# Optimization experiments

Measured on AMD Instinct MI355X. Metric: run time of the kernel, lower is better.

The kernel has to match this reference:

```python
import jax, jax.numpy as jnp
import numpy as np

B, S, D, H, NH = 4, 4096, 256, 1024, 8


def _layernorm(x, g, b, eps=1e-5):
    mu = jnp.mean(x, axis=-1, keepdims=True)
    var = jnp.var(x, axis=-1, keepdims=True)
    return (x - mu) / jnp.sqrt(var + eps) * g + b


def setup_inputs() -> dict:
    key = jax.random.key(0)
    ks = jax.random.split(key, 3)
    std = 0.02
    return {
        "x": jax.random.normal(ks[0], (B, S, D), dtype=jnp.float32),
        "gamma1": jnp.ones((D,), jnp.float32),
        "beta1": jnp.zeros((D,), jnp.float32),
        "W1": jax.random.normal(ks[1], (D, H), dtype=jnp.float32) * std,
        "b1": jnp.zeros((H,), jnp.float32),
        "W2": jax.random.normal(ks[2], (H, D), dtype=jnp.float32) * std,
        "b2": jnp.zeros((D,), jnp.float32),
        "gamma2": jnp.ones((D,), jnp.float32),
        "beta2": jnp.zeros((D,), jnp.float32),
        "n_head": NH,
    }


def reference(x, gamma1, beta1, W1, b1, W2, b2, gamma2, beta2, n_head):
    # First-call path of CachedLocalMultiheadAttention: single-head softmax
    # attention on raw x, scale = (d_model // n_head) ** -0.5, no masks.
    scale = (x.shape[-1] // n_head) ** -0.5
    scores = jnp.einsum('bqd,bkd->bqk', x, x) * scale  # [B,S,S]
    attn = jax.nn.softmax(scores, axis=-1)
    a = jnp.einsum('bqk,bkd->bqd', attn, x)
    # residual + LayerNorm (dropouts are identity in eval)
    h = _layernorm(a + x, gamma1, beta1)
    # positionwise FFN
    f = jnp.maximum(h @ W1 + b1, 0.0) @ W2 + b2
    return _layernorm(f + h, gamma2, beta2)
```

## Files before the change

kernel.cpp:

```cpp
#include <hip/hip_runtime.h>


#define DIM 256
#define SEQ 4096
#define BATCHN 4
#define HID 1024
#define NROW (BATCHN * SEQ)

typedef __attribute__((ext_vector_type(8))) short short8;
typedef __attribute__((ext_vector_type(4))) float float4v;
typedef __attribute__((ext_vector_type(16))) float float16v;

static __device__ __forceinline__ unsigned int f2bf1(float f) {
  unsigned int b = __float_as_uint(f);
  return (b + 0x7fffu + ((b >> 16) & 1u)) >> 16;
}
static __device__ __forceinline__ unsigned int pack2bf(float lo, float hi) {
  return f2bf1(lo) | (f2bf1(hi) << 16);
}
static __device__ __forceinline__ float bf2f(unsigned short v) {
  return __uint_as_float(((unsigned int)v) << 16);
}
static __device__ __forceinline__ float bflo(unsigned int p) { return __uint_as_float(p << 16); }
static __device__ __forceinline__ float bfhi(unsigned int p) { return __uint_as_float(p & 0xffff0000u); }

static __device__ __forceinline__ void bar_lgkm() {
  __asm__ __volatile__("s_waitcnt lgkmcnt(0)" ::: "memory");
  __builtin_amdgcn_s_barrier();
  __asm__ __volatile__("" ::: "memory");
}

__global__ __launch_bounds__(256, 2) void attn_part(
    const float* __restrict__ x,
    unsigned short* __restrict__ P01, unsigned short* __restrict__ P23,
    float* __restrict__ lpart) {
  __shared__ unsigned short Krow[32][264];
  __shared__ unsigned short Vt[256][40];
  __shared__ unsigned short Pbuf[4][32][40];

  const int tid = threadIdx.x;
  const int w = tid >> 6;
  const int l = tid & 63;
  const int n = l & 31;
  const int half = l >> 5;
  const int b = blockIdx.y;
  const int z = blockIdx.z;
  const int qw = (blockIdx.x << 7) + (w << 5);
  const float* xb = x + (size_t)b * SEQ * DIM;
  const float scale = 0.17677669529663687f;
  const float SHIFT = 46.0f;

  short8 qf[16];
#pragma unroll
  for (int c = 0; c < 16; c++) {
    const float* qp = xb + (size_t)(qw + n) * DIM + (c << 4) + (half << 3);
    float4 a0 = *reinterpret_cast<const float4*>(qp);
    float4 a1 = *reinterpret_cast<const float4*>(qp + 4);
    short8 q8;
    q8[0] = (short)f2bf1(a0.x); q8[1] = (short)f2bf1(a0.y);
    q8[2] = (short)f2bf1(a0.z); q8[3] = (short)f2bf1(a0.w);
    q8[4] = (short)f2bf1(a1.x); q8[5] = (short)f2bf1(a1.y);
    q8[6] = (short)f2bf1(a1.z); q8[7] = (short)f2bf1(a1.w);
    qf[c] = q8;
  }

  float16v o[8];
#pragma unroll
  for (int nb = 0; nb < 8; nb++)
#pragma unroll
    for (int r = 0; r < 16; r++) o[nb][r] = 0.f;
  float lsum = 0.f;

  const int skey = tid & 31;
  const int sd = (tid >> 5) << 5;
  const int kbase = z << 10;

  float4 ld0[4];
  {
    const float* sp = xb + (size_t)(kbase + skey) * DIM + sd;
#pragma unroll
    for (int j = 0; j < 4; j++) ld0[j] = *reinterpret_cast<const float4*>(sp + (j << 2));
  }

  for (int k0 = kbase; k0 < kbase + 1024; k0 += 32) {
    const float* sp = xb + (size_t)(k0 + skey) * DIM + sd;
    float4 ld1[4];
#pragma unroll
    for (int j = 0; j < 4; j++) ld1[j] = *reinterpret_cast<const float4*>(sp + 16 + (j << 2));

    bar_lgkm();
#pragma unroll
    for (int j = 0; j < 4; j++)
      *reinterpret_cast<uint2*>(&Krow[skey][sd + (j << 2)]) =
          make_uint2(pack2bf(ld0[j].x, ld0[j].y), pack2bf(ld0[j].z, ld0[j].w));
#pragma unroll
    for (int j = 0; j < 4; j++)
      *reinterpret_cast<uint2*>(&Krow[skey][sd + 16 + (j << 2)]) =
          make_uint2(pack2bf(ld1[j].x, ld1[j].y), pack2bf(ld1[j].z, ld1[j].w));
#pragma unroll
    for (int j = 0; j < 4; j++) {
      Vt[sd + (j << 2) + 0][skey] = (unsigned short)f2bf1(ld0[j].x);
      Vt[sd + (j << 2) + 1][skey] = (unsigned short)f2bf1(ld0[j].y);
      Vt[sd + (j << 2) + 2][skey] = (unsigned short)f2bf1(ld0[j].z);
      Vt[sd + (j << 2) + 3][skey] = (unsigned short)f2bf1(ld0[j].w);
    }
#pragma unroll
    for (int j = 0; j < 4; j++) {
      Vt[sd + 16 + (j << 2) + 0][skey] = (unsigned short)f2bf1(ld1[j].x);
      Vt[sd + 16 + (j << 2) + 1][skey] = (unsigned short)f2bf1(ld1[j].y);
      Vt[sd + 16 + (j << 2) + 2][skey] = (unsigned short)f2bf1(ld1[j].z);
      Vt[sd + 16 + (j << 2) + 3][skey] = (unsigned short)f2bf1(ld1[j].w);
    }
    bar_lgkm();

    {
      const int kn = (k0 + 32 < kbase + 1024) ? (k0 + 32) : k0;
      const float* spn = xb + (size_t)(kn + skey) * DIM + sd;
#pragma unroll
      for (int j = 0; j < 4; j++) ld0[j] = *reinterpret_cast<const float4*>(spn + (j << 2));
    }

    float16v s;
#pragma unroll
    for (int r = 0; r < 16; r++) s[r] = 0.f;
#pragma unroll
    for (int c = 0; c < 16; c++) {
      short8 a = *reinterpret_cast<const short8*>(&Krow[n][(c << 4) + (half << 3)]);
      s = __builtin_amdgcn_mfma_f32_32x32x16_bf16(a, qf[c], s, 0, 0, 0);
    }
#pragma unroll
    for (int g = 0; g < 4; g++) {
      float p0 = __expf(fmaf(s[(g << 2) + 0], scale, -SHIFT));
      float p1 = __expf(fmaf(s[(g << 2) + 1], scale, -SHIFT));
      float p2 = __expf(fmaf(s[(g << 2) + 2], scale, -SHIFT));
      float p3 = __expf(fmaf(s[(g << 2) + 3], scale, -SHIFT));
      lsum += (p0 + p1) + (p2 + p3);
      *reinterpret_cast<uint2*>(&Pbuf[w][n][(g << 3) + (half << 2)]) =
          make_uint2(pack2bf(p0, p1), pack2bf(p2, p3));
    }
    __asm__ __volatile__("" ::: "memory");

#pragma unroll
    for (int kk = 0; kk < 2; kk++) {
      short8 pf = *reinterpret_cast<const short8*>(&Pbuf[w][n][(kk << 4) + (half << 3)]);
#pragma unroll
      for (int nb = 0; nb < 8; nb++) {
        short8 vf = *reinterpret_cast<const short8*>(&Vt[(nb << 5) + n][(kk << 4) + (half << 3)]);
        o[nb] = __builtin_amdgcn_mfma_f32_32x32x16_bf16(pf, vf, o[nb], 0, 0, 0);
      }
    }
  }

  lsum += __shfl_xor(lsum, 32);
  if (l < 32) lpart[(z << 14) + (b << 12) + qw + l] = lsum;

  unsigned short* Op = ((z < 2) ? P01 : P23) + ((size_t)(z & 1) << 22);
#pragma unroll
  for (int nb = 0; nb < 8; nb++) {
#pragma unroll
    for (int r = 0; r < 16; r++) {
      const int q = (r & 3) + ((r >> 2) << 3) + (half << 2);
      Op[((size_t)(b << 12) + qw + q) * DIM + (nb << 5) + n] = (unsigned short)f2bf1(o[nb][r]);
    }
  }
}

__global__ __launch_bounds__(256) void merge_ln1(
    const unsigned short* __restrict__ P01, const unsigned short* __restrict__ P23,
    const float* __restrict__ lpart, const float* __restrict__ x,
    const float* __restrict__ g1, const float* __restrict__ be1,
    unsigned short* __restrict__ hbf) {
  const int tid = threadIdx.x;
  const int row = (blockIdx.x << 5) + (tid >> 3);
  const int c0 = (tid & 7) << 5;
  const float rl = 1.0f / (lpart[row] + lpart[NROW + row] +
                           lpart[2 * NROW + row] + lpart[3 * NROW + row]);
  const float* px = x + (size_t)row * DIM + c0;

  float v[32];
#pragma unroll
  for (int j = 0; j < 32; j++) v[j] = 0.f;
#pragma unroll
  for (int part = 0; part < 4; part++) {
    const unsigned short* pb = ((part < 2) ? P01 : P23) + ((size_t)(part & 1) << 22) +
                               (size_t)row * DIM + c0;
#pragma unroll
    for (int j = 0; j < 8; j++) {
      uint2 raw = *reinterpret_cast<const uint2*>(pb + (j << 2));
      v[(j << 2) + 0] += bflo(raw.x); v[(j << 2) + 1] += bfhi(raw.x);
      v[(j << 2) + 2] += bflo(raw.y); v[(j << 2) + 3] += bfhi(raw.y);
    }
  }
#pragma unroll
  for (int j = 0; j < 8; j++) {
    float4 xr = *reinterpret_cast<const float4*>(px + (j << 2));
    v[(j << 2) + 0] = fmaf(v[(j << 2) + 0], rl, xr.x);
    v[(j << 2) + 1] = fmaf(v[(j << 2) + 1], rl, xr.y);
    v[(j << 2) + 2] = fmaf(v[(j << 2) + 2], rl, xr.z);
    v[(j << 2) + 3] = fmaf(v[(j << 2) + 3], rl, xr.w);
  }
  float s = 0.f, s2 = 0.f;
#pragma unroll
  for (int j = 0; j < 32; j++) { s += v[j]; s2 = fmaf(v[j], v[j], s2); }
  s += __shfl_xor(s, 1); s += __shfl_xor(s, 2); s += __shfl_xor(s, 4);
  s2 += __shfl_xor(s2, 1); s2 += __shfl_xor(s2, 2); s2 += __shfl_xor(s2, 4);
  const float mean = s * (1.f / 256.f);
  const float var = s2 * (1.f / 256.f) - mean * mean;
  const float rstd = rsqrtf(var + 1e-5f);
  unsigned short* hb = hbf + (size_t)row * DIM + c0;
  unsigned int pk[16];
#pragma unroll
  for (int j = 0; j < 8; j++) {
    float4 gv = *reinterpret_cast<const float4*>(g1 + c0 + (j << 2));
    float4 bv = *reinterpret_cast<const float4*>(be1 + c0 + (j << 2));
    float o0 = fmaf((v[(j << 2) + 0] - mean) * rstd, gv.x, bv.x);
    float o1 = fmaf((v[(j << 2) + 1] - mean) * rstd, gv.y, bv.y);
    float o2 = fmaf((v[(j << 2) + 2] - mean) * rstd, gv.z, bv.z);
    float o3 = fmaf((v[(j << 2) + 3] - mean) * rstd, gv.w, bv.w);
    pk[2 * j] = pack2bf(o0, o1); pk[2 * j + 1] = pack2bf(o2, o3);
  }
#pragma unroll
  for (int q = 0; q < 4; q++)
    *reinterpret_cast<uint4*>(hb + (q << 3)) =
        make_uint4(pk[4 * q], pk[4 * q + 1], pk[4 * q + 2], pk[4 * q + 3]);
}

__global__ __launch_bounds__(256) void prep_w(
    const float* __restrict__ W1, const float* __restrict__ W2,
    unsigned short* __restrict__ W1Tb, unsigned short* __restrict__ W2Tb) {
  __shared__ float Ls[64][65];
  const int tid = threadIdx.x;
  const bool second = blockIdx.x >= 64;
  const int bid = blockIdx.x - (second ? 64 : 0);
  const int N = second ? DIM : HID;
  const float* src = second ? W2 : W1;
  unsigned short* dst = second ? W2Tb : W1Tb;
  const int ntn = N >> 6;
  const int k0 = (bid / ntn) << 6, n0 = (bid % ntn) << 6;

  const int r = tid >> 2, cg = (tid & 3) << 4;
#pragma unroll
  for (int q = 0; q < 4; q++) {
    float4 v = *reinterpret_cast<const float4*>(src + (size_t)(k0 + r) * N + n0 + cg + (q << 2));
    Ls[r][cg + (q << 2) + 0] = v.x; Ls[r][cg + (q << 2) + 1] = v.y;
    Ls[r][cg + (q << 2) + 2] = v.z; Ls[r][cg + (q << 2) + 3] = v.w;
  }
  __syncthreads();
  const int j = tid >> 2, part = tid & 3;
  const int kbl = part >> 1, ko = (part & 1) << 4, kl = part << 4;
  unsigned int pk[8];
#pragma unroll
  for (int q = 0; q < 8; q++) pk[q] = pack2bf(Ls[kl + 2 * q][j], Ls[kl + 2 * q + 1][j]);
  unsigned short* dp = dst + (((size_t)((k0 >> 5) + kbl) * N + n0 + j) << 5) + ko;
  *reinterpret_cast<uint4*>(dp) = make_uint4(pk[0], pk[1], pk[2], pk[3]);
  *reinterpret_cast<uint4*>(dp + 8) = make_uint4(pk[4], pk[5], pk[6], pk[7]);
}

__global__ __launch_bounds__(256) void ffn1_mfma(
    const unsigned short* __restrict__ hbf, const unsigned short* __restrict__ W1Tb,
    const float* __restrict__ b1, unsigned short* __restrict__ ub) {
  __shared__ unsigned short As[128][264];
  __shared__ unsigned short Bs[128][40];
  const int tid = threadIdx.x;
  const int w = tid >> 6;
  const int l = tid & 63;
  const int tx = l & 15;
  const int p = l >> 4;
  const int wm = w >> 1, wn = w & 1;
  const int r0 = blockIdx.x << 7, c0 = blockIdx.y << 7;

  float4v acc[4][4];
#pragma unroll
  for (int i = 0; i < 4; i++)
#pragma unroll
    for (int j = 0; j < 4; j++) acc[i][j] = (float4v){0.f, 0.f, 0.f, 0.f};

  {
    const unsigned short* base = hbf + (size_t)r0 * DIM;
#pragma unroll
    for (int j = 0; j < 16; j++) {
      const int fo = (tid << 3) + (j << 11);
      uint4 v = *reinterpret_cast<const uint4*>(base + fo);
      *reinterpret_cast<uint4*>(&As[fo >> 8][fo & 255]) = v;
    }
  }
  for (int kb = 0; kb < 8; kb++) {
    __syncthreads();
    {
      const unsigned short* base = W1Tb + (((size_t)kb * HID + c0) << 5);
#pragma unroll
      for (int j = 0; j < 2; j++) {
        const int fo = (tid << 3) + (j << 11);
        uint4 v = *reinterpret_cast<const uint4*>(base + fo);
        *reinterpret_cast<uint4*>(&Bs[fo >> 5][fo & 31]) = v;
      }
    }
    __syncthreads();
    short8 af[4], bf[4];
#pragma unroll
    for (int f = 0; f < 4; f++) {
      af[f] = *reinterpret_cast<const short8*>(&As[(wm << 6) + (f << 4) + tx][(kb << 5) + (p << 3)]);
      bf[f] = *reinterpret_cast<const short8*>(&Bs[(wn << 6) + (f << 4) + tx][p << 3]);
    }
#pragma unroll
    for (int i = 0; i < 4; i++)
#pragma unroll
      for (int j = 0; j < 4; j++)
        acc[i][j] = __builtin_amdgcn_mfma_f32_16x16x32_bf16(af[i], bf[j], acc[i][j], 0, 0, 0);
  }
  float bias[4];
#pragma unroll
  for (int j = 0; j < 4; j++) bias[j] = b1[c0 + (wn << 6) + (j << 4) + tx];
  __syncthreads();
  unsigned short (*Ep)[72] = reinterpret_cast<unsigned short(*)[72]>(&As[0][0] + w * 2304);
#pragma unroll
  for (int hh = 0; hh < 2; hh++) {
#pragma unroll
    for (int i2 = 0; i2 < 2; i2++) {
      const int i = (hh << 1) + i2;
#pragma unroll
      for (int j = 0; j < 4; j++)
#pragma unroll
        for (int rg = 0; rg < 4; rg++)
          Ep[(i2 << 4) + (p << 2) + rg][(j << 4) + tx] =
              (unsigned short)f2bf1(fmaxf(acc[i][j][rg] + bias[j], 0.f));
    }
    __syncthreads();
    const int cb = l >> 5, r32 = l & 31;
    const int grow = r0 + (wm << 6) + (hh << 5) + r32;
    const int kb = (c0 >> 5) + (wn << 1) + cb;
    unsigned short* up = ub + (((size_t)kb * NROW + grow) << 5);
#pragma unroll
    for (int q = 0; q < 4; q++)
      *reinterpret_cast<uint4*>(up + (q << 3)) =
          *reinterpret_cast<const uint4*>(&Ep[r32][(cb << 5) + (q << 3)]);
    __syncthreads();
  }
}

__global__ __launch_bounds__(256) void ffn2_mfma(
    const unsigned short* __restrict__ ub, const unsigned short* __restrict__ W2Tb,
    const float* __restrict__ b2, const unsigned short* __restrict__ hbf,
    const float* __restrict__ g2, const float* __restrict__ be2,
    float* __restrict__ out) {
  __shared__ unsigned short As[32][40];
  __shared__ unsigned short Bs[256][40];
  __shared__ float2 red[32][4];
  const int tid = threadIdx.x;
  const int w = tid >> 6;
  const int l = tid & 63;
  const int tx = l & 15;
  const int p = l >> 4;
  const int r0 = blockIdx.x << 5;

  float4v acc[2][4];
#pragma unroll
  for (int i = 0; i < 2; i++)
#pragma unroll
    for (int j = 0; j < 4; j++) acc[i][j] = (float4v){0.f, 0.f, 0.f, 0.f};

  for (int kb = 0; kb < 32; kb++) {
    __syncthreads();
    if (tid < 128) {
      const int fo = tid << 3;
      uint4 v = *reinterpret_cast<const uint4*>(ub + (((size_t)kb * NROW + r0) << 5) + fo);
      *reinterpret_cast<uint4*>(&As[fo >> 5][fo & 31]) = v;
    }
    {
      const unsigned short* base = W2Tb + (((size_t)kb * DIM) << 5);
#pragma unroll
      for (int j = 0; j < 4; j++) {
        const int fo = (tid << 3) + (j << 11);
        uint4 v = *reinterpret_cast<const uint4*>(base + fo);
        *reinterpret_cast<uint4*>(&Bs[fo >> 5][fo & 31]) = v;
      }
    }
    __syncthreads();
    short8 af[2], bf[4];
#pragma unroll
    for (int i = 0; i < 2; i++)
      af[i] = *reinterpret_cast<const short8*>(&As[(i << 4) + tx][p << 3]);
#pragma unroll
    for (int j = 0; j < 4; j++)
      bf[j] = *reinterpret_cast<const short8*>(&Bs[(w << 6) + (j << 4) + tx][p << 3]);
#pragma unroll
    for (int i = 0; i < 2; i++)
#pragma unroll
      for (int j = 0; j < 4; j++)
        acc[i][j] = __builtin_amdgcn_mfma_f32_16x16x32_bf16(af[i], bf[j], acc[i][j], 0, 0, 0);
  }

  float bias[4];
#pragma unroll
  for (int j = 0; j < 4; j++) bias[j] = b2[(w << 6) + (j << 4) + tx];
#pragma unroll
  for (int i = 0; i < 2; i++)
#pragma unroll
    for (int rg = 0; rg < 4; rg++) {
      const int row = r0 + (i << 4) + (p << 2) + rg;
#pragma unroll
      for (int j = 0; j < 4; j++)
        acc[i][j][rg] += bias[j] + bf2f(hbf[(size_t)row * DIM + (w << 6) + (j << 4) + tx]);
    }
#pragma unroll
  for (int i = 0; i < 2; i++)
#pragma unroll
    for (int rg = 0; rg < 4; rg++) {
      float s = acc[i][0][rg] + acc[i][1][rg] + acc[i][2][rg] + acc[i][3][rg];
      float s2 = 0.f;
#pragma unroll
      for (int j = 0; j < 4; j++) s2 = fmaf(acc[i][j][rg], acc[i][j][rg], s2);
      s += __shfl_xor(s, 1); s += __shfl_xor(s, 2);
      s += __shfl_xor(s, 4); s += __shfl_xor(s, 8);
      s2 += __shfl_xor(s2, 1); s2 += __shfl_xor(s2, 2);
      s2 += __shfl_xor(s2, 4); s2 += __shfl_xor(s2, 8);
      if (tx == 0) red[(i << 4) + (p << 2) + rg][w] = make_float2(s, s2);
    }
  __syncthreads();
#pragma unroll
  for (int i = 0; i < 2; i++)
#pragma unroll
    for (int rg = 0; rg < 4; rg++) {
      const int rl = (i << 4) + (p << 2) + rg;
      float2 a0 = red[rl][0], a1 = red[rl][1], a2 = red[rl][2], a3 = red[rl][3];
      const float S = (a0.x + a1.x) + (a2.x + a3.x);
      const float S2 = (a0.y + a1.y) + (a2.y + a3.y);
      const float mean = S * (1.f / 256.f);
      const float var = S2 * (1.f / 256.f) - mean * mean;
      const float rstd = rsqrtf(var + 1e-5f);
      const int row = r0 + rl;
#pragma unroll
      for (int j = 0; j < 4; j++) {
        const int col = (w << 6) + (j << 4) + tx;
        out[(size_t)row * DIM + col] =
            fmaf((acc[i][j][rg] - mean) * rstd, g2[col], be2[col]);
      }
    }
}

extern "C" void kernel_launch(void* const* d_in, const int* in_sizes, int n_in,
                              void* d_out, int out_size, void* d_ws, size_t ws_size,
                              hipStream_t stream) {
  const float* x = (const float*)d_in[0];
  const float* g1 = (const float*)d_in[1];
  const float* be1 = (const float*)d_in[2];
  const float* W1 = (const float*)d_in[3];
  const float* b1 = (const float*)d_in[4];
  const float* W2 = (const float*)d_in[5];
  const float* b2 = (const float*)d_in[6];
  const float* g2 = (const float*)d_in[7];
  const float* be2 = (const float*)d_in[8];
  float* out = (float*)d_out;
  char* wsb = (char*)d_ws;

  unsigned short* P01 = (unsigned short*)d_out;
  unsigned short* P23 = (unsigned short*)wsb;
  float* lp = (float*)(wsb + ((size_t)16 << 20));
  unsigned short* u = (unsigned short*)wsb;
  unsigned short* hbf = (unsigned short*)(wsb + ((size_t)32 << 20));
  unsigned short* W2Tb = (unsigned short*)(wsb + ((size_t)40 << 20));
  unsigned short* W1Tb = (unsigned short*)d_out;

  attn_part<<<dim3(SEQ / 128, BATCHN, 4), 256, 0, stream>>>(x, P01, P23, lp);
  merge_ln1<<<dim3(NROW / 32), 256, 0, stream>>>(P01, P23, lp, x, g1, be1, hbf);
  prep_w<<<dim3(128), 256, 0, stream>>>(W1, W2, W1Tb, W2Tb);
  ffn1_mfma<<<dim3(NROW / 128, HID / 128), 256, 0, stream>>>(hbf, W1Tb, b1, u);
  ffn2_mfma<<<dim3(NROW / 32), 256, 0, stream>>>(u, W2Tb, b2, hbf, g2, be2, out);
}
```

Baseline: 256.4 us.

## Keep softmax P in registers via permlane32 swap, pair-key V staging, fuse weight prep

The attention kernel no longer round-trips the probability tile through shared memory. It packs P to bf16 in registers and uses v_permlane32_swap to rearrange it into the MFMA A-operand layout. K/V staging now has each thread load two adjacent keys, so the transposed V writes become packed 32-bit stores instead of 16-bit scalar stores. The weight transpose/convert kernel is merged into the merge+LayerNorm launch as extra blocks, and W1Tb moves to workspace so it no longer aliases the output buffer. This removes a kernel launch and LDS traffic, at the cost of relying on an inline-asm lane permutation being correct for the fragment layout.

After: 243.5 us. -5.0%, faster.

```diff
diff --git a/kernel.cpp b/kernel.cpp
--- a/kernel.cpp
+++ b/kernel.cpp
@@ -29,6 +29,12 @@
   __builtin_amdgcn_s_barrier();
   __asm__ __volatile__("" ::: "memory");
 }
+
+static __device__ __forceinline__ void pl32swap(unsigned int& a, unsigned int& b) {
+  __asm__ __volatile__("v_permlane32_swap_b32 %0, %1" : "+v"(a), "+v"(b));
+}
+
+union FragU { uint4 u; short8 s; };
 
 __global__ __launch_bounds__(256, 2) void attn_part(
     const float* __restrict__ x,
@@ -36,16 +42,14 @@
     float* __restrict__ lpart) {
   __shared__ unsigned short Krow[32][264];
   __shared__ unsigned short Vt[256][40];
-  __shared__ unsigned short Pbuf[4][32][40];
 
   const int tid = threadIdx.x;
-  const int w = tid >> 6;
   const int l = tid & 63;
   const int n = l & 31;
   const int half = l >> 5;
   const int b = blockIdx.y;
   const int z = blockIdx.z;
-  const int qw = (blockIdx.x << 7) + (w << 5);
+  const int qw = (blockIdx.x << 7) + ((tid >> 6) << 5);
   const float* xb = x + (size_t)b * SEQ * DIM;
   const float scale = 0.17677669529663687f;
   const float SHIFT = 46.0f;
@@ -71,53 +75,48 @@
     for (int r = 0; r < 16; r++) o[nb][r] = 0.f;
   float lsum = 0.f;
 
-  const int skey = tid & 31;
-  const int sd = (tid >> 5) << 5;
+  const int kp = tid & 15;
+  const int sd2 = (tid >> 4) << 4;
   const int kbase = z << 10;
 
-  float4 ld0[4];
+  float4 e0[4];
   {
-    const float* sp = xb + (size_t)(kbase + skey) * DIM + sd;
-#pragma unroll
-    for (int j = 0; j < 4; j++) ld0[j] = *reinterpret_cast<const float4*>(sp + (j << 2));
+    const float* sp = xb + (size_t)(kbase + (kp << 1)) * DIM + sd2;
+#pragma unroll
+    for (int j = 0; j < 4; j++) e0[j] = *reinterpret_cast<const float4*>(sp + (j << 2));
   }
 
   for (int k0 = kbase; k0 < kbase + 1024; k0 += 32) {
-    const float* sp = xb + (size_t)(k0 + skey) * DIM + sd;
-    float4 ld1[4];
-#pragma unroll
-    for (int j = 0; j < 4; j++) ld1[j] = *reinterpret_cast<const float4*>(sp + 16 + (j << 2));
+    float4 e1[4];
+    {
+      const float* sp = xb + (size_t)(k0 + (kp << 1) + 1) * DIM + sd2;
+#pragma unroll
+      for (int j = 0; j < 4; j++) e1[j] = *reinterpret_cast<const float4*>(sp + (j << 2));
+    }
 
     bar_lgkm();
 #pragma unroll
-    for (int j = 0; j < 4; j++)
-      *reinterpret_cast<uint2*>(&Krow[skey][sd + (j << 2)]) =
-          make_uint2(pack2bf(ld0[j].x, ld0[j].y), pack2bf(ld0[j].z, ld0[j].w));
-#pragma unroll
-    for (int j = 0; j < 4; j++)
-      *reinterpret_cast<uint2*>(&Krow[skey][sd + 16 + (j << 2)]) =
-          make_uint2(pack2bf(ld1[j].x, ld1[j].y), pack2bf(ld1[j].z, ld1[j].w));
-#pragma unroll
     for (int j = 0; j < 4; j++) {
-      Vt[sd + (j << 2) + 0][skey] = (unsigned short)f2bf1(ld0[j].x);
-      Vt[sd + (j << 2) + 1][skey] = (unsigned short)f2bf1(ld0[j].y);
-      Vt[sd + (j << 2) + 2][skey] = (unsigned short)f2bf1(ld0[j].z);
-      Vt[sd + (j << 2) + 3][skey] = (unsigned short)f2bf1(ld0[j].w);
+      *reinterpret_cast<uint2*>(&Krow[(kp << 1) + 0][sd2 + (j << 2)]) =
+          make_uint2(pack2bf(e0[j].x, e0[j].y), pack2bf(e0[j].z, e0[j].w));
+      *reinterpret_cast<uint2*>(&Krow[(kp << 1) + 1][sd2 + (j << 2)]) =
+          make_uint2(pack2bf(e1[j].x, e1[j].y), pack2bf(e1[j].z, e1[j].w));
     }
 #pragma unroll
     for (int j = 0; j < 4; j++) {
-      Vt[sd + 16 + (j << 2) + 0][skey] = (unsigned short)f2bf1(ld1[j].x);
-      Vt[sd + 16 + (j << 2) + 1][skey] = (unsigned short)f2bf1(ld1[j].y);
-      Vt[sd + 16 + (j << 2) + 2][skey] = (unsigned short)f2bf1(ld1[j].z);
-      Vt[sd + 16 + (j << 2) + 3][skey] = (unsigned short)f2bf1(ld1[j].w);
+      const int d = sd2 + (j << 2);
+      *reinterpret_cast<unsigned int*>(&Vt[d + 0][kp << 1]) = pack2bf(e0[j].x, e1[j].x);
+      *reinterpret_cast<unsigned int*>(&Vt[d + 1][kp << 1]) = pack2bf(e0[j].y, e1[j].y);
+      *reinterpret_cast<unsigned int*>(&Vt[d + 2][kp << 1]) = pack2bf(e0[j].z, e1[j].z);
+      *reinterpret_cast<unsigned int*>(&Vt[d + 3][kp << 1]) = pack2bf(e0[j].w, e1[j].w);
     }
     bar_lgkm();
 
     {
       const int kn = (k0 + 32 < kbase + 1024) ? (k0 + 32) : k0;
-      const float* spn = xb + (size_t)(kn + skey) * DIM + sd;
-#pragma unroll
-      for (int j = 0; j < 4; j++) ld0[j] = *reinterpret_cast<const float4*>(spn + (j << 2));
+      const float* spn = xb + (size_t)(kn + (kp << 1)) * DIM + sd2;
+#pragma unroll
+      for (int j = 0; j < 4; j++) e0[j] = *reinterpret_cast<const float4*>(spn + (j << 2));
     }
 
     float16v s;
@@ -128,21 +127,27 @@
       short8 a = *reinterpret_cast<const short8*>(&Krow[n][(c << 4) + (half << 3)]);
       s = __builtin_amdgcn_mfma_f32_32x32x16_bf16(a, qf[c], s, 0, 0, 0);
     }
+    float p[16];
+#pragma unroll
+    for (int r = 0; r < 16; r++) {
+      p[r] = __expf(fmaf(s[r], scale, -SHIFT));
+      lsum += p[r];
+    }
+    unsigned int Pr[8];
 #pragma unroll
     for (int g = 0; g < 4; g++) {
-      float p0 = __expf(fmaf(s[(g << 2) + 0], scale, -SHIFT));
-      float p1 = __expf(fmaf(s[(g << 2) + 1], scale, -SHIFT));
-      float p2 = __expf(fmaf(s[(g << 2) + 2], scale, -SHIFT));
-      float p3 = __expf(fmaf(s[(g << 2) + 3], scale, -SHIFT));
-      lsum += (p0 + p1) + (p2 + p3);
-      *reinterpret_cast<uint2*>(&Pbuf[w][n][(g << 3) + (half << 2)]) =
-          make_uint2(pack2bf(p0, p1), pack2bf(p2, p3));
-    }
-    __asm__ __volatile__("" ::: "memory");
+      Pr[2 * g + 0] = pack2bf(p[4 * g + 0], p[4 * g + 1]);
+      Pr[2 * g + 1] = pack2bf(p[4 * g + 2], p[4 * g + 3]);
+    }
+    pl32swap(Pr[0], Pr[2]); pl32swap(Pr[1], Pr[3]);
+    pl32swap(Pr[4], Pr[6]); pl32swap(Pr[5], Pr[7]);
+    FragU f0, f1;
+    f0.u = make_uint4(Pr[0], Pr[1], Pr[2], Pr[3]);
+    f1.u = make_uint4(Pr[4], Pr[5], Pr[6], Pr[7]);
 
 #pragma unroll
     for (int kk = 0; kk < 2; kk++) {
-      short8 pf = *reinterpret_cast<const short8*>(&Pbuf[w][n][(kk << 4) + (half << 3)]);
+      const short8 pf = kk ? f1.s : f0.s;
 #pragma unroll
       for (int nb = 0; nb < 8; nb++) {
         short8 vf = *reinterpret_cast<const short8*>(&Vt[(nb << 5) + n][(kk << 4) + (half << 3)]);
@@ -165,12 +170,43 @@
   }
 }
 
-__global__ __launch_bounds__(256) void merge_ln1(
+__global__ __launch_bounds__(256) void merge_prep(
     const unsigned short* __restrict__ P01, const unsigned short* __restrict__ P23,
     const float* __restrict__ lpart, const float* __restrict__ x,
     const float* __restrict__ g1, const float* __restrict__ be1,
-    unsigned short* __restrict__ hbf) {
+    unsigned short* __restrict__ hbf,
+    const float* __restrict__ W1, const float* __restrict__ W2,
+    unsigned short* __restrict__ W1Tb, unsigned short* __restrict__ W2Tb) {
+  __shared__ float Ls[64][65];
   const int tid = threadIdx.x;
+  if (blockIdx.x >= 512) {
+    const int bid = blockIdx.x - 512;
+    const bool second = bid >= 64;
+    const int wid = bid - (second ? 64 : 0);
+    const int N = second ? DIM : HID;
+    const float* src = second ? W2 : W1;
+    unsigned short* dst = second ? W2Tb : W1Tb;
+    const int ntn = N >> 6;
+    const int k0 = (wid / ntn) << 6, n0 = (wid % ntn) << 6;
+
+    const int r = tid >> 2, cg = (tid & 3) << 4;
+#pragma unroll
+    for (int q = 0; q < 4; q++) {
+      float4 v = *reinterpret_cast<const float4*>(src + (size_t)(k0 + r) * N + n0 + cg + (q << 2));
+      Ls[r][cg + (q << 2) + 0] = v.x; Ls[r][cg + (q << 2) + 1] = v.y;
+      Ls[r][cg + (q << 2) + 2] = v.z; Ls[r][cg + (q << 2) + 3] = v.w;
+    }
+    __syncthreads();
+    const int j = tid >> 2, part = tid & 3;
+    const int kbl = part >> 1, ko = (part & 1) << 4, kl = part << 4;
+    unsigned int pk[8];
+#pragma unroll
+    for (int q = 0; q < 8; q++) pk[q] = pack2bf(Ls[kl + 2 * q][j], Ls[kl + 2 * q + 1][j]);
+    unsigned short* dp = dst + (((size_t)((k0 >> 5) + kbl) * N + n0 + j) << 5) + ko;
+    *reinterpret_cast<uint4*>(dp) = make_uint4(pk[0], pk[1], pk[2], pk[3]);
+    *reinterpret_cast<uint4*>(dp + 8) = make_uint4(pk[4], pk[5], pk[6], pk[7]);
+    return;
+  }
   const int row = (blockIdx.x << 5) + (tid >> 3);
   const int c0 = (tid & 7) << 5;
   const float rl = 1.0f / (lpart[row] + lpart[NROW + row] +
@@ -223,37 +259,6 @@
   for (int q = 0; q < 4; q++)
     *reinterpret_cast<uint4*>(hb + (q << 3)) =
         make_uint4(pk[4 * q], pk[4 * q + 1], pk[4 * q + 2], pk[4 * q + 3]);
-}
-
-__global__ __launch_bounds__(256) void prep_w(
-    const float* __restrict__ W1, const float* __restrict__ W2,
-    unsigned short* __restrict__ W1Tb, unsigned short* __restrict__ W2Tb) {
-  __shared__ float Ls[64][65];
-  const int tid = threadIdx.x;
-  const bool second = blockIdx.x >= 64;
-  const int bid = blockIdx.x - (second ? 64 : 0);
-  const int N = second ? DIM : HID;
-  const float* src = second ? W2 : W1;
-  unsigned short* dst = second ? W2Tb : W1Tb;
-  const int ntn = N >> 6;
-  const int k0 = (bid / ntn) << 6, n0 = (bid % ntn) << 6;
-
-  const int r = tid >> 2, cg = (tid & 3) << 4;
-#pragma unroll
-  for (int q = 0; q < 4; q++) {
-    float4 v = *reinterpret_cast<const float4*>(src + (size_t)(k0 + r) * N + n0 + cg + (q << 2));
-    Ls[r][cg + (q << 2) + 0] = v.x; Ls[r][cg + (q << 2) + 1] = v.y;
-    Ls[r][cg + (q << 2) + 2] = v.z; Ls[r][cg + (q << 2) + 3] = v.w;
-  }
-  __syncthreads();
-  const int j = tid >> 2, part = tid & 3;
-  const int kbl = part >> 1, ko = (part & 1) << 4, kl = part << 4;
-  unsigned int pk[8];
-#pragma unroll
-  for (int q = 0; q < 8; q++) pk[q] = pack2bf(Ls[kl + 2 * q][j], Ls[kl + 2 * q + 1][j]);
-  unsigned short* dp = dst + (((size_t)((k0 >> 5) + kbl) * N + n0 + j) << 5) + ko;
-  *reinterpret_cast<uint4*>(dp) = make_uint4(pk[0], pk[1], pk[2], pk[3]);
-  *reinterpret_cast<uint4*>(dp + 8) = make_uint4(pk[4], pk[5], pk[6], pk[7]);
 }
 
 __global__ __launch_bounds__(256) void ffn1_mfma(
@@ -459,11 +464,11 @@
   unsigned short* u = (unsigned short*)wsb;
   unsigned short* hbf = (unsigned short*)(wsb + ((size_t)32 << 20));
   unsigned short* W2Tb = (unsigned short*)(wsb + ((size_t)40 << 20));
-  unsigned short* W1Tb = (unsigned short*)d_out;
+  unsigned short* W1Tb = (unsigned short*)(wsb + ((size_t)40 << 20) + ((size_t)512 << 10));
 
   attn_part<<<dim3(SEQ / 128, BATCHN, 4), 256, 0, stream>>>(x, P01, P23, lp);
-  merge_ln1<<<dim3(NROW / 32), 256, 0, stream>>>(P01, P23, lp, x, g1, be1, hbf);
-  prep_w<<<dim3(128), 256, 0, stream>>>(W1, W2, W1Tb, W2Tb);
+  merge_prep<<<dim3(512 + 128), 256, 0, stream>>>(P01, P23, lp, x, g1, be1, hbf,
+                                                  W1, W2, W1Tb, W2Tb);
   ffn1_mfma<<<dim3(NROW / 128, HID / 128), 256, 0, stream>>>(hbf, W1Tb, b1, u);
   ffn2_mfma<<<dim3(NROW / 32), 256, 0, stream>>>(u, W2Tb, b2, hbf, g2, be2, out);
 }
```
